# Performance work log

Hardware: AMD Instinct MI355X
Metric: run time of the kernel (lower is better)

The kernel has to match this reference:

```python
import jax, jax.numpy as jnp
import numpy as np

B = 1_048_576
NUM_ITERS = 10  # training-mode default; eval mode uses 1000
EPS = 1e-12
LOW, HIGH = 0.02, 0.98  # SquashedSigmoid bounds


def setup_inputs() -> dict:
    key = jax.random.key(0)
    ks = jax.random.split(key, 4)
    # margins are population masses -> keep strictly positive
    margins = jax.random.uniform(ks[0], (B, 8), dtype=jnp.float32) + 0.1

    def lin(k, i, o):
        return (jax.random.normal(k, (i, o), jnp.float32) / np.sqrt(i)).astype(jnp.float32)

    return {
        "margins": margins,
        "W1": lin(ks[1], 8, 32), "b1": jnp.zeros((32,), jnp.float32),
        "W2": lin(ks[2], 32, 16), "b2": jnp.zeros((16,), jnp.float32),
        "W3": lin(ks[3], 16, 9), "b3": jnp.zeros((9,), jnp.float32),
    }


def tau_batched(p):
    # p: (B,4) positive params -> (B,3,3) positive couples matrix.
    # 2x2 core, extended by geometric-mean row/col (user-supplied tau in repo).
    a = p.reshape(-1, 2, 2)
    col3 = jnp.sqrt(a[:, :, 0] * a[:, :, 1])          # (B,2)
    row3 = jnp.sqrt(a[:, 0, :] * a[:, 1, :])          # (B,2)
    corner = jnp.sqrt(row3[:, 0] * row3[:, 1])        # (B,)
    top = jnp.concatenate([a, col3[:, :, None]], axis=2)                 # (B,2,3)
    bot = jnp.concatenate([row3, corner[:, None]], axis=1)[:, None, :]   # (B,1,3)
    return jnp.concatenate([top, bot], axis=1)        # (B,3,3)


def sinkhorn_knopp(A, row_margins, col_margins, iters):
    # Batched Sinkhorn-Knopp: A (B,R,C), row_margins (B,R), col_margins (B,C)
    r = row_margins[:, :, None]
    c = col_margins[:, None, :]

    def body(A, _):
        A = A * (r / (A.sum(axis=2, keepdims=True) + EPS))
        A = A * (c / (A.sum(axis=1, keepdims=True) + EPS))
        return A, None

    A, _ = jax.lax.scan(body, A, None, length=iters)
    return A


def reference(margins, W1, b1, W2, b2, W3, b3):
    Bn = margins.shape[0]
    M, F = margins[:, 0:3], margins[:, 3:6]

    # MLP: Linear-ReLU-Linear-ReLU-Linear
    h = jax.nn.relu(margins @ W1 + b1)
    h = jax.nn.relu(h @ W2 + b2)
    pars = h @ W3 + b3                                   # (B,9)

    muc = tau_batched(jnp.exp(pars[:, 0:4]))             # (B,3,3)
    sqs = lambda x: LOW + (HIGH - LOW) * jax.nn.sigmoid(x)
    shm, shf = sqs(pars[:, 4:6]), sqs(pars[:, 6:8])      # (B,2) each
    V = jnp.exp(pars[:, -1])                             # (B,)

    ones = jnp.ones((Bn, 1), margins.dtype)
    shm0 = jnp.concatenate([shm, ones], axis=1)          # (B,3)
    shf0 = jnp.concatenate([shf, ones], axis=1)          # (B,3)
    mucm0, muc0f = M * shm0, F * shf0                    # matched masses (margins)
    mum0, mu0f = M * (1.0 - shm0), F * (1.0 - shf0)      # singles

    muc = sinkhorn_knopp(muc, mucm0, muc0f, NUM_ITERS)   # (B,3,3)

    top = jnp.concatenate([muc, mum0[:, :, None]], axis=2)   # (B,3,4)
    bot = jnp.concatenate(
        [mu0f[:, None, :], jnp.zeros((Bn, 1, 1), margins.dtype)], axis=2)  # (B,1,4)
    mus = jnp.concatenate([top, bot], axis=1)            # (B,4,4)
    return mus, V
```

## Files before the change

kernel.cpp:

```cpp
#include <hip/hip_runtime.h>
#include <math.h>


#define QLOW  0.02f
#define QSPAN 0.96f
#define L2E   1.44269504088896f

typedef __attribute__((ext_vector_type(2))) float f32x2;

__device__ __forceinline__ float frcp(float x) { return __builtin_amdgcn_rcpf(x); }
__device__ __forceinline__ f32x2 pfma(f32x2 a, f32x2 b, f32x2 c) {
    return __builtin_elementwise_fma(a, b, c);
}

__global__ __launch_bounds__(256) void sinkhorn_fused(
    const float* __restrict__ margins,
    const float* __restrict__ W1, const float* __restrict__ b1,
    const float* __restrict__ W2, const float* __restrict__ b2,
    const float* __restrict__ W3, const float* __restrict__ b3,
    float* __restrict__ out, int n)
{
    __shared__ __align__(16) float sW1[256];
    __shared__ __align__(16) float sW2[512];
    __shared__ __align__(16) float sW3[16 * 12];
    __shared__ __align__(16) float sB1[32];
    __shared__ __align__(16) float sB2[16];
    __shared__ __align__(16) float sB3[12];

    {
        const int t = threadIdx.x;
        sW1[t] = W1[t];
        sW2[t] = W2[t];
        sW2[t + 256] = W2[t + 256];
        if (t < 144) { const int k = t / 9, j = t - 9 * k; sW3[k * 12 + j] = W3[t]; }
        if (t < 32) sB1[t] = b1[t];
        if (t < 16) sB2[t] = b2[t];
        if (t < 9)  sB3[t] = b3[t];
    }
    __syncthreads();

    const float4* __restrict__ sW1q = (const float4*)sW1;
    const float4* __restrict__ sW2q = (const float4*)sW2;
    const float4* __restrict__ sW3q = (const float4*)sW3;

    const int row = blockIdx.x * blockDim.x + threadIdx.x;

    const float4* __restrict__ m4 = (const float4*)margins;
    const float4 a0 = m4[row * 2 + 0];
    const float4 a1 = m4[row * 2 + 1];
    float m[8];
    m[0] = a0.x; m[1] = a0.y; m[2] = a0.z; m[3] = a0.w;
    m[4] = a1.x; m[5] = a1.y; m[6] = a1.z; m[7] = a1.w;

    f32x2 h1[16];
#pragma unroll
    for (int j = 0; j < 16; ++j) { h1[j].x = sB1[2 * j]; h1[j].y = sB1[2 * j + 1]; }
#pragma unroll
    for (int k = 0; k < 8; ++k) {
        f32x2 mk; mk.x = m[k]; mk.y = m[k];
#pragma unroll
        for (int j4 = 0; j4 < 8; ++j4) {
            const float4 w = sW1q[k * 8 + j4];
            const f32x2 wa = {w.x, w.y};
            const f32x2 wb = {w.z, w.w};
            h1[2 * j4 + 0] = pfma(mk, wa, h1[2 * j4 + 0]);
            h1[2 * j4 + 1] = pfma(mk, wb, h1[2 * j4 + 1]);
        }
    }
    const f32x2 zero2 = {0.0f, 0.0f};
#pragma unroll
    for (int j = 0; j < 16; ++j) h1[j] = __builtin_elementwise_max(h1[j], zero2);

    f32x2 h2[8];
#pragma unroll
    for (int j = 0; j < 8; ++j) { h2[j].x = sB2[2 * j]; h2[j].y = sB2[2 * j + 1]; }
#pragma unroll
    for (int k = 0; k < 32; ++k) {
        const float s = (k & 1) ? h1[k >> 1].y : h1[k >> 1].x;
        f32x2 hk; hk.x = s; hk.y = s;
#pragma unroll
        for (int j4 = 0; j4 < 4; ++j4) {
            const float4 w = sW2q[k * 4 + j4];
            const f32x2 wa = {w.x, w.y};
            const f32x2 wb = {w.z, w.w};
            h2[2 * j4 + 0] = pfma(hk, wa, h2[2 * j4 + 0]);
            h2[2 * j4 + 1] = pfma(hk, wb, h2[2 * j4 + 1]);
        }
    }
#pragma unroll
    for (int j = 0; j < 8; ++j) h2[j] = __builtin_elementwise_max(h2[j], zero2);

    f32x2 p01 = {sB3[0], sB3[1]};
    f32x2 p23 = {sB3[2], sB3[3]};
    f32x2 p45 = {sB3[4], sB3[5]};
    f32x2 p67 = {sB3[6], sB3[7]};
    float p8 = sB3[8];
#pragma unroll
    for (int k = 0; k < 16; ++k) {
        const float4 wA = sW3q[k * 3 + 0];
        const float4 wB = sW3q[k * 3 + 1];
        const float w8  = sW3[k * 12 + 8];
        const float s = (k & 1) ? h2[k >> 1].y : h2[k >> 1].x;
        f32x2 hb; hb.x = s; hb.y = s;
        p01 = pfma(hb, (f32x2){wA.x, wA.y}, p01);
        p23 = pfma(hb, (f32x2){wA.z, wA.w}, p23);
        p45 = pfma(hb, (f32x2){wB.x, wB.y}, p45);
        p67 = pfma(hb, (f32x2){wB.z, wB.w}, p67);
        p8  = fmaf(s, w8, p8);
    }

    const float l0 = p01.x * L2E, l1 = p01.y * L2E;
    const float l2 = p23.x * L2E, l3 = p23.y * L2E;

    const float a00 = exp2f(l0), a01 = exp2f(l1);
    const float a10 = exp2f(l2), a11 = exp2f(l3);
    const float h01 = (l0 + l1) * 0.5f, h23 = (l2 + l3) * 0.5f;
    const float a02 = exp2f(h01);
    const float a12 = exp2f(h23);
    const float a20 = exp2f((l0 + l2) * 0.5f);
    const float a21 = exp2f((l1 + l3) * 0.5f);
    const float a22 = exp2f((h01 + h23) * 0.5f);

    const float s4 = fmaf(QSPAN, frcp(1.0f + exp2f(-L2E * p45.x)), QLOW);
    const float s5 = fmaf(QSPAN, frcp(1.0f + exp2f(-L2E * p45.y)), QLOW);
    const float s6 = fmaf(QSPAN, frcp(1.0f + exp2f(-L2E * p67.x)), QLOW);
    const float s7 = fmaf(QSPAN, frcp(1.0f + exp2f(-L2E * p67.y)), QLOW);

    const float M0 = m[0], M1 = m[1], M2 = m[2];
    const float F0 = m[3], F1 = m[4], F2 = m[5];

    const float rm0 = M0 * s4, rm1 = M1 * s5, rm2 = M2;
    const float cm0 = F0 * s6, cm1 = F1 * s7, cm2 = F2;
    const float um0 = fmaf(-s4, M0, M0);
    const float um1 = fmaf(-s5, M1, M1);
    const float uf0 = fmaf(-s6, F0, F0);
    const float uf1 = fmaf(-s7, F1, F1);

    const float B00 = a00 * rm0, B01 = a01 * rm0, B02 = a02 * rm0;
    const float B10 = a10 * rm1, B11 = a11 * rm1, B12 = a12 * rm1;
    const float B20 = a20 * rm2, B21 = a21 * rm2, B22 = a22 * rm2;
    const float C00 = a00 * cm0, C01 = a01 * cm1, C02 = a02 * cm2;
    const float C10 = a10 * cm0, C11 = a11 * cm1, C12 = a12 * cm2;
    const float C20 = a20 * cm0, C21 = a21 * cm1, C22 = a22 * cm2;

    float t0 = (a00 + a01) + a02;
    float t1 = (a10 + a11) + a12;
    float t2 = (a20 + a21) + a22;
    float z0, z1, z2, w0, w1, w2;
#pragma unroll
    for (int it = 0; it < 10; ++it) {
        z0 = frcp(t0); z1 = frcp(t1); z2 = frcp(t2);
        const float q0 = fmaf(B20, z2, fmaf(B10, z1, B00 * z0));
        const float q1 = fmaf(B21, z2, fmaf(B11, z1, B01 * z0));
        const float q2 = fmaf(B22, z2, fmaf(B12, z1, B02 * z0));
        w0 = frcp(q0); w1 = frcp(q1); w2 = frcp(q2);
        if (it < 9) {
            t0 = fmaf(C02, w2, fmaf(C01, w1, C00 * w0));
            t1 = fmaf(C12, w2, fmaf(C11, w1, C10 * w0));
            t2 = fmaf(C22, w2, fmaf(C21, w1, C20 * w0));
        }
    }
    const float u0 = rm0 * z0, u1 = rm1 * z1, u2 = rm2 * z2;

    const float A0f = u0 * C00 * w0, A1f = u0 * C01 * w1, A2f = u0 * C02 * w2;
    const float A3f = u1 * C10 * w0, A4f = u1 * C11 * w1, A5f = u1 * C12 * w2;
    const float A6f = u2 * C20 * w0, A7f = u2 * C21 * w1, A8f = u2 * C22 * w2;

    float4* __restrict__ o4 = (float4*)out;
    float* __restrict__ oV = out + (size_t)n * 16;

    o4[row * 4 + 0] = make_float4(A0f, A1f, A2f, um0);
    o4[row * 4 + 1] = make_float4(A3f, A4f, A5f, um1);
    o4[row * 4 + 2] = make_float4(A6f, A7f, A8f, 0.0f);
    o4[row * 4 + 3] = make_float4(uf0, uf1, 0.0f, 0.0f);
    oV[row] = exp2f(p8 * L2E);
}

extern "C" void kernel_launch(void* const* d_in, const int* in_sizes, int n_in,
                              void* d_out, int out_size, void* d_ws, size_t ws_size,
                              hipStream_t stream) {
    const float* margins = (const float*)d_in[0];
    const float* W1 = (const float*)d_in[1];
    const float* b1 = (const float*)d_in[2];
    const float* W2 = (const float*)d_in[3];
    const float* b2 = (const float*)d_in[4];
    const float* W3 = (const float*)d_in[5];
    const float* b3 = (const float*)d_in[6];

    const int n = in_sizes[0] / 8;
    dim3 block(256), grid(n / 256);

    sinkhorn_fused<<<grid, block, 0, stream>>>(margins, W1, b1, W2, b2, W3, b3,
                                               (float*)d_out, n);
}
```

Measured before the change: 136.9 us.

## Read MLP weights via uniform global loads and cut Sinkhorn register pressure

Removes the shared-memory staging of the MLP weights and the block-wide barrier. Weights and biases are now read straight from global memory through wave-uniform addresses, which the compiler can turn into scalar loads. The Sinkhorn loop folds the margin scalings into the rcp products, so the 18 precomputed B/C coefficients are no longer kept live. The launch bound also asks for 8 blocks per CU. The aim is to lower VGPR use and LDS traffic and so raise occupancy. The risk is that weights go through the scalar cache, and the occupancy hint may force spills.

```diff
diff --git a/kernel.cpp b/kernel.cpp
--- a/kernel.cpp
+++ b/kernel.cpp
@@ -13,99 +13,74 @@
     return __builtin_elementwise_fma(a, b, c);
 }
 
-__global__ __launch_bounds__(256) void sinkhorn_fused(
+__global__ __launch_bounds__(256, 8) void sinkhorn_fused(
     const float* __restrict__ margins,
     const float* __restrict__ W1, const float* __restrict__ b1,
     const float* __restrict__ W2, const float* __restrict__ b2,
     const float* __restrict__ W3, const float* __restrict__ b3,
     float* __restrict__ out, int n)
 {
-    __shared__ __align__(16) float sW1[256];
-    __shared__ __align__(16) float sW2[512];
-    __shared__ __align__(16) float sW3[16 * 12];
-    __shared__ __align__(16) float sB1[32];
-    __shared__ __align__(16) float sB2[16];
-    __shared__ __align__(16) float sB3[12];
-
-    {
-        const int t = threadIdx.x;
-        sW1[t] = W1[t];
-        sW2[t] = W2[t];
-        sW2[t + 256] = W2[t + 256];
-        if (t < 144) { const int k = t / 9, j = t - 9 * k; sW3[k * 12 + j] = W3[t]; }
-        if (t < 32) sB1[t] = b1[t];
-        if (t < 16) sB2[t] = b2[t];
-        if (t < 9)  sB3[t] = b3[t];
-    }
-    __syncthreads();
-
-    const float4* __restrict__ sW1q = (const float4*)sW1;
-    const float4* __restrict__ sW2q = (const float4*)sW2;
-    const float4* __restrict__ sW3q = (const float4*)sW3;
-
     const int row = blockIdx.x * blockDim.x + threadIdx.x;
 
     const float4* __restrict__ m4 = (const float4*)margins;
-    const float4 a0 = m4[row * 2 + 0];
-    const float4 a1 = m4[row * 2 + 1];
+    const float4 a0q = m4[row * 2 + 0];
+    const float4 a1q = m4[row * 2 + 1];
     float m[8];
-    m[0] = a0.x; m[1] = a0.y; m[2] = a0.z; m[3] = a0.w;
-    m[4] = a1.x; m[5] = a1.y; m[6] = a1.z; m[7] = a1.w;
+    m[0] = a0q.x; m[1] = a0q.y; m[2] = a0q.z; m[3] = a0q.w;
+    m[4] = a1q.x; m[5] = a1q.y; m[6] = a1q.z; m[7] = a1q.w;
+
+    const f32x2* __restrict__ W1v = (const f32x2*)W1;
+    const f32x2* __restrict__ W2v = (const f32x2*)W2;
+    const f32x2* __restrict__ b1v = (const f32x2*)b1;
+    const f32x2* __restrict__ b2v = (const f32x2*)b2;
+
+    const f32x2 zero2 = {0.0f, 0.0f};
 
     f32x2 h1[16];
 #pragma unroll
-    for (int j = 0; j < 16; ++j) { h1[j].x = sB1[2 * j]; h1[j].y = sB1[2 * j + 1]; }
+    for (int j = 0; j < 16; ++j) h1[j] = b1v[j];
 #pragma unroll
     for (int k = 0; k < 8; ++k) {
         f32x2 mk; mk.x = m[k]; mk.y = m[k];
 #pragma unroll
-        for (int j4 = 0; j4 < 8; ++j4) {
-            const float4 w = sW1q[k * 8 + j4];
-            const f32x2 wa = {w.x, w.y};
-            const f32x2 wb = {w.z, w.w};
-            h1[2 * j4 + 0] = pfma(mk, wa, h1[2 * j4 + 0]);
-            h1[2 * j4 + 1] = pfma(mk, wb, h1[2 * j4 + 1]);
-        }
+        for (int j = 0; j < 16; ++j)
+            h1[j] = pfma(mk, W1v[k * 16 + j], h1[j]);
     }
-    const f32x2 zero2 = {0.0f, 0.0f};
 #pragma unroll
     for (int j = 0; j < 16; ++j) h1[j] = __builtin_elementwise_max(h1[j], zero2);
 
     f32x2 h2[8];
 #pragma unroll
-    for (int j = 0; j < 8; ++j) { h2[j].x = sB2[2 * j]; h2[j].y = sB2[2 * j + 1]; }
+    for (int j = 0; j < 8; ++j) h2[j] = b2v[j];
 #pragma unroll
     for (int k = 0; k < 32; ++k) {
         const float s = (k & 1) ? h1[k >> 1].y : h1[k >> 1].x;
         f32x2 hk; hk.x = s; hk.y = s;
 #pragma unroll
-        for (int j4 = 0; j4 < 4; ++j4) {
-            const float4 w = sW2q[k * 4 + j4];
-            const f32x2 wa = {w.x, w.y};
-            const f32x2 wb = {w.z, w.w};
-            h2[2 * j4 + 0] = pfma(hk, wa, h2[2 * j4 + 0]);
-            h2[2 * j4 + 1] = pfma(hk, wb, h2[2 * j4 + 1]);
-        }
+        for (int j = 0; j < 8; ++j)
+            h2[j] = pfma(hk, W2v[k * 8 + j], h2[j]);
     }
 #pragma unroll
     for (int j = 0; j < 8; ++j) h2[j] = __builtin_elementwise_max(h2[j], zero2);
 
-    f32x2 p01 = {sB3[0], sB3[1]};
-    f32x2 p23 = {sB3[2], sB3[3]};
-    f32x2 p45 = {sB3[4], sB3[5]};
-    f32x2 p67 = {sB3[6], sB3[7]};
-    float p8 = sB3[8];
+    f32x2 p01 = {b3[0], b3[1]};
+    f32x2 p23 = {b3[2], b3[3]};
+    f32x2 p45 = {b3[4], b3[5]};
+    f32x2 p67 = {b3[6], b3[7]};
+    float p8 = b3[8];
 #pragma unroll
     for (int k = 0; k < 16; ++k) {
-        const float4 wA = sW3q[k * 3 + 0];
-        const float4 wB = sW3q[k * 3 + 1];
-        const float w8  = sW3[k * 12 + 8];
+        const f32x2 w01 = {W3[k * 9 + 0], W3[k * 9 + 1]};
+        const f32x2 w23 = {W3[k * 9 + 2], W3[k * 9 + 3]};
+        const f32x2 w45 = {W3[k * 9 + 4], W3[k * 9 + 5]};
+        const f32x2 w67 = {W3[k * 9 + 6], W3[k * 9 + 7]};
+        const float w8  = W3[k * 9 + 8];
         const float s = (k & 1) ? h2[k >> 1].y : h2[k >> 1].x;
         f32x2 hb; hb.x = s; hb.y = s;
-        p01 = pfma(hb, (f32x2){wA.x, wA.y}, p01);
-        p23 = pfma(hb, (f32x2){wA.z, wA.w}, p23);
-        p45 = pfma(hb, (f32x2){wB.x, wB.y}, p45);
-        p67 = pfma(hb, (f32x2){wB.z, wB.w}, p67);
+        p01 = pfma(hb, w01, p01);
+        p23 = pfma(hb, w23, p23);
+        p45 = pfma(hb, w45, p45);
+        p67 = pfma(hb, w67, p67);
         p8  = fmaf(s, w8, p8);
     }
 
@@ -126,45 +101,40 @@
     const float s6 = fmaf(QSPAN, frcp(1.0f + exp2f(-L2E * p67.x)), QLOW);
     const float s7 = fmaf(QSPAN, frcp(1.0f + exp2f(-L2E * p67.y)), QLOW);
 
-    const float M0 = m[0], M1 = m[1], M2 = m[2];
-    const float F0 = m[3], F1 = m[4], F2 = m[5];
-
-    const float rm0 = M0 * s4, rm1 = M1 * s5, rm2 = M2;
-    const float cm0 = F0 * s6, cm1 = F1 * s7, cm2 = F2;
-    const float um0 = fmaf(-s4, M0, M0);
-    const float um1 = fmaf(-s5, M1, M1);
-    const float uf0 = fmaf(-s6, F0, F0);
-    const float uf1 = fmaf(-s7, F1, F1);
-
-    const float B00 = a00 * rm0, B01 = a01 * rm0, B02 = a02 * rm0;
-    const float B10 = a10 * rm1, B11 = a11 * rm1, B12 = a12 * rm1;
-    const float B20 = a20 * rm2, B21 = a21 * rm2, B22 = a22 * rm2;
-    const float C00 = a00 * cm0, C01 = a01 * cm1, C02 = a02 * cm2;
-    const float C10 = a10 * cm0, C11 = a11 * cm1, C12 = a12 * cm2;
-    const float C20 = a20 * cm0, C21 = a21 * cm1, C22 = a22 * cm2;
+    const float rm0 = m[0] * s4, rm1 = m[1] * s5, rm2 = m[2];
+    const float cm0 = m[3] * s6, cm1 = m[4] * s7, cm2 = m[5];
 
     float t0 = (a00 + a01) + a02;
     float t1 = (a10 + a11) + a12;
     float t2 = (a20 + a21) + a22;
-    float z0, z1, z2, w0, w1, w2;
+
+    float zp0, zp1, zp2, wp0, wp1, wp2;
 #pragma unroll
     for (int it = 0; it < 10; ++it) {
-        z0 = frcp(t0); z1 = frcp(t1); z2 = frcp(t2);
-        const float q0 = fmaf(B20, z2, fmaf(B10, z1, B00 * z0));
-        const float q1 = fmaf(B21, z2, fmaf(B11, z1, B01 * z0));
-        const float q2 = fmaf(B22, z2, fmaf(B12, z1, B02 * z0));
-        w0 = frcp(q0); w1 = frcp(q1); w2 = frcp(q2);
+        zp0 = rm0 * frcp(t0);
+        zp1 = rm1 * frcp(t1);
+        zp2 = rm2 * frcp(t2);
+        const float q0 = fmaf(a20, zp2, fmaf(a10, zp1, a00 * zp0));
+        const float q1 = fmaf(a21, zp2, fmaf(a11, zp1, a01 * zp0));
+        const float q2 = fmaf(a22, zp2, fmaf(a12, zp1, a02 * zp0));
+        wp0 = cm0 * frcp(q0);
+        wp1 = cm1 * frcp(q1);
+        wp2 = cm2 * frcp(q2);
         if (it < 9) {
-            t0 = fmaf(C02, w2, fmaf(C01, w1, C00 * w0));
-            t1 = fmaf(C12, w2, fmaf(C11, w1, C10 * w0));
-            t2 = fmaf(C22, w2, fmaf(C21, w1, C20 * w0));
+            t0 = fmaf(a02, wp2, fmaf(a01, wp1, a00 * wp0));
+            t1 = fmaf(a12, wp2, fmaf(a11, wp1, a10 * wp0));
+            t2 = fmaf(a22, wp2, fmaf(a21, wp1, a20 * wp0));
         }
     }
-    const float u0 = rm0 * z0, u1 = rm1 * z1, u2 = rm2 * z2;
 
-    const float A0f = u0 * C00 * w0, A1f = u0 * C01 * w1, A2f = u0 * C02 * w2;
-    const float A3f = u1 * C10 * w0, A4f = u1 * C11 * w1, A5f = u1 * C12 * w2;
-    const float A6f = u2 * C20 * w0, A7f = u2 * C21 * w1, A8f = u2 * C22 * w2;
+    const float A0f = zp0 * a00 * wp0, A1f = zp0 * a01 * wp1, A2f = zp0 * a02 * wp2;
+    const float A3f = zp1 * a10 * wp0, A4f = zp1 * a11 * wp1, A5f = zp1 * a12 * wp2;
+    const float A6f = zp2 * a20 * wp0, A7f = zp2 * a21 * wp1, A8f = zp2 * a22 * wp2;
+
+    const float um0 = m[0] - rm0;
+    const float um1 = m[1] - rm1;
+    const float uf0 = m[3] - cm0;
+    const float uf1 = m[4] - cm1;
 
     float4* __restrict__ o4 = (float4*)out;
     float* __restrict__ oV = out + (size_t)n * 16;
```

Measured after the change: 129.8 us. 1.05x faster.
